# Kernel tuning notes

Measured on AMD Instinct MI355X. Metric: run time of the kernel, lower is better.

Reference implementation:

```python
import jax, jax.numpy as jnp
import numpy as np

N_HEAD = 16
N_EMBD = 1024

def setup_inputs() -> dict:
    key = jax.random.key(0)
    ks = jax.random.split(key, 5)
    C = N_EMBD
    x = jax.random.normal(ks[0], (4, 2048, C), dtype=jnp.float32)
    s = 1.0 / np.sqrt(C)
    W_attn = jax.random.normal(ks[1], (C, 3 * C), dtype=jnp.float32) * s
    b_attn = jax.random.normal(ks[2], (3 * C,), dtype=jnp.float32) * 0.02
    W_proj = jax.random.normal(ks[3], (C, C), dtype=jnp.float32) * s
    b_proj = jax.random.normal(ks[4], (C,), dtype=jnp.float32) * 0.02
    return {"x": x, "W_attn": W_attn, "b_attn": b_attn, "W_proj": W_proj, "b_proj": b_proj}

def reference(x, W_attn, b_attn, W_proj, b_proj):
    B, T, C = x.shape
    H = C // N_HEAD
    qkv = x @ W_attn + b_attn  # [B,T,3C]
    q, k, v = jnp.split(qkv, 3, axis=2)
    # [B,T,C] -> [B,nh,T,H]
    q = q.reshape(B, T, N_HEAD, H).transpose(0, 2, 1, 3)
    k = k.reshape(B, T, N_HEAD, H).transpose(0, 2, 1, 3)
    v = v.reshape(B, T, N_HEAD, H).transpose(0, 2, 1, 3)
    att = jnp.einsum('bhqd,bhkd->bhqk', q, k) * (1.0 / np.sqrt(H).astype(np.float32))
    causal = jnp.tril(jnp.ones((T, T), dtype=bool))  # [T,T]
    att = jnp.where(causal, att, -jnp.inf)
    att = jax.nn.softmax(att, axis=-1)
    y = jnp.einsum('bhqk,bhkd->bhqd', att, v)
    y = y.transpose(0, 2, 1, 3).reshape(B, T, C)
    return y @ W_proj + b_proj
```

## Files before the change

kernel.cpp:

```cpp
#include <hip/hip_runtime.h>
#include <math.h>

#define T_LEN 2048
#define C_DIM 1024
#define C3    3072
#define NHEAD 16
#define HDIM  64

typedef __attribute__((ext_vector_type(8))) __bf16 bf16x8;
typedef __attribute__((ext_vector_type(8))) unsigned short u16x8;
typedef __attribute__((ext_vector_type(4))) float f32x4;
typedef __attribute__((ext_vector_type(2))) unsigned int u32x2;
typedef unsigned short ushort_t;

#define QK_SCALE 0.180336878f

#if defined(__has_builtin)
#if __has_builtin(__builtin_amdgcn_exp2f)
#define FAST_EXP2(x) __builtin_amdgcn_exp2f(x)
#endif
#if __has_builtin(__builtin_amdgcn_permlane32_swap) && __has_builtin(__builtin_amdgcn_permlane16_swap)
#define HAVE_PERMLANE_SWAP 1
#endif
#endif
#ifndef FAST_EXP2
#define FAST_EXP2(x) exp2f(x)
#endif

__device__ __forceinline__ ushort_t f2bf(float f) {
    unsigned int u = __float_as_uint(f);
    unsigned int r = (u + 0x7FFFu + ((u >> 16) & 1u)) >> 16;
    return (ushort_t)r;
}

#define GLL16(g, l) __builtin_amdgcn_global_load_lds( \
    (const __attribute__((address_space(1))) void*)(g), \
    (__attribute__((address_space(3))) void*)(l), 16, 0, 0)

__global__ __launch_bounds__(256) void prep_inputs(
    const float* __restrict__ x, ushort_t* __restrict__ xb,
    const float* __restrict__ W1, ushort_t* __restrict__ Wt1,
    const float* __restrict__ W2, ushort_t* __restrict__ Wt2)
{
    __shared__ float t[64][65];
    const int bx = blockIdx.x;
    if (bx < 8192) {
        const int i = bx * 256 + threadIdx.x;
        const float4 v = ((const float4*)x)[i];
        ushort4 o;
        o.x = f2bf(v.x); o.y = f2bf(v.y); o.z = f2bf(v.z); o.w = f2bf(v.w);
        ((ushort4*)xb)[i] = o;
        return;
    }
    const float* W; ushort_t* Wt; int N, n0, k0;
    if (bx < 8960) {
        const int tt = bx - 8192;
        W = W1; Wt = Wt1; N = C3;
        n0 = (tt % 48) * 64; k0 = (tt / 48) * 64;
    } else {
        const int tt = bx - 8960;
        W = W2; Wt = Wt2; N = C_DIM;
        n0 = (tt % 16) * 64; k0 = (tt / 16) * 64;
    }
    const int K = C_DIM;
    const int c = threadIdx.x & 63, r4 = threadIdx.x >> 6;
#pragma unroll
    for (int i = 0; i < 16; i++) {
        int r = i * 4 + r4;
        t[r][c] = W[(size_t)(k0 + r) * N + n0 + c];
    }
    __syncthreads();
#pragma unroll
    for (int i = 0; i < 16; i++) {
        int r = i * 4 + r4;
        Wt[(size_t)(n0 + r) * K + k0 + c] = f2bf(t[c][r]);
    }
}

template <bool OUT_BF16, bool QSCALE>
__global__ __launch_bounds__(256, 3) void gemm_bt_mfma(
    const ushort_t* __restrict__ A, const ushort_t* __restrict__ Bt,
    const float* __restrict__ bias, void* __restrict__ Cv,
    int M, int N, int K)
{
    __shared__ ushort_t Alds[128 * 64];
    __shared__ ushort_t Blds[128 * 64];

    const int tid = threadIdx.x;
    const int m0 = blockIdx.y * 128;
    const int n0 = blockIdx.x * 128;
    const int w = tid >> 6;
    const int ln = tid & 63;
    const int quad = ln >> 4;
    const int r16 = ln & 15;
    const int wr0 = (w & 1) * 64;
    const int wc0 = (w >> 1) * 64;

    f32x4 acc[4][4] = {};

    const int srow = tid >> 3;
    const int csrc8 = ((tid & 7) ^ (srow & 7)) * 8;
    const int sw = r16 & 7;

    for (int k0 = 0; k0 < K; k0 += 64) {
#pragma unroll
        for (int rr = 0; rr < 4; rr++) {
            const ushort_t* ga = A + (size_t)(m0 + rr * 32 + srow) * K + k0 + csrc8;
            GLL16(ga, Alds + rr * 2048 + tid * 8);
            const ushort_t* gb = Bt + (size_t)(n0 + rr * 32 + srow) * K + k0 + csrc8;
            GLL16(gb, Blds + rr * 2048 + tid * 8);
        }
        __syncthreads();

#pragma unroll
        for (int s = 0; s < 2; s++) {
            const int cpos = ((4 * s + quad) ^ sw) * 8;
            bf16x8 af[4], bfr[4];
#pragma unroll
            for (int i = 0; i < 4; i++)
                af[i] = *(const bf16x8*)(Alds + (wr0 + i * 16 + r16) * 64 + cpos);
#pragma unroll
            for (int j = 0; j < 4; j++)
                bfr[j] = *(const bf16x8*)(Blds + (wc0 + j * 16 + r16) * 64 + cpos);
#pragma unroll
            for (int i = 0; i < 4; i++)
#pragma unroll
                for (int j = 0; j < 4; j++)
                    acc[i][j] = __builtin_amdgcn_mfma_f32_16x16x32_bf16(
                        af[i], bfr[j], acc[i][j], 0, 0, 0);
        }
        __syncthreads();
    }

    const float scl = (QSCALE && n0 < C_DIM) ? QK_SCALE : 1.0f;

#pragma unroll
    for (int j = 0; j < 4; j++) {
        const int col = n0 + wc0 + j * 16 + r16;
        const float bv = bias[col];
#pragma unroll
        for (int i = 0; i < 4; i++) {
            const int rowb = m0 + wr0 + i * 16 + quad * 4;
#pragma unroll
            for (int r = 0; r < 4; r++) {
                const float v = (acc[i][j][r] + bv) * scl;
                if (OUT_BF16)
                    ((ushort_t*)Cv)[(size_t)(rowb + r) * N + col] = f2bf(v);
                else
                    ((float*)Cv)[(size_t)(rowb + r) * N + col] = v;
            }
        }
    }
}

__global__ __launch_bounds__(256) void transpose_v(
    const ushort_t* __restrict__ qkv, ushort_t* __restrict__ vtg)
{
    __shared__ ushort_t Ts[64][72];
    const int t0 = blockIdx.x * 64;
    const int bh = blockIdx.y;
    const int b = bh >> 4, h = bh & 15;
    const ushort_t* src = qkv + (size_t)b * T_LEN * C3 + 2 * C_DIM + h * HDIM;
    const int tid = threadIdx.x;
    {
        const int r = tid >> 2, cs = (tid & 3) * 16;
        *(u16x8*)(&Ts[r][cs])     = *(const u16x8*)(src + (size_t)(t0 + r) * C3 + cs);
        *(u16x8*)(&Ts[r][cs + 8]) = *(const u16x8*)(src + (size_t)(t0 + r) * C3 + cs + 8);
    }
    __syncthreads();
    {
        const int d = tid >> 2, ts0 = (tid & 3) * 16;
        ushort_t* dst = vtg + ((size_t)bh * HDIM + d) * T_LEN + t0 + ts0;
        u16x8 o0, o1;
#pragma unroll
        for (int j = 0; j < 8; j++) o0[j] = Ts[ts0 + j][d];
#pragma unroll
        for (int j = 0; j < 8; j++) o1[j] = Ts[ts0 + 8 + j][d];
        *(u16x8*)dst = o0;
        *(u16x8*)(dst + 8) = o1;
    }
}


__device__ __forceinline__ void mask_diag(f32x4 (&s)[4], int qloc, int quad)
{
#pragma unroll
    for (int mb = 0; mb < 4; mb++)
#pragma unroll
        for (int r = 0; r < 4; r++)
            if (mb * 16 + quad * 4 + r > qloc) s[mb][r] = -1e30f;
}

__device__ __forceinline__ void softmax_exchange(
    f32x4 (&s)[4], float& lacc, bf16x8 (&bp)[2])
{
    unsigned int pk[4][2];
#pragma unroll
    for (int mb = 0; mb < 4; mb++) {
        const float p0 = FAST_EXP2(s[mb][0]);
        const float p1 = FAST_EXP2(s[mb][1]);
        const float p2 = FAST_EXP2(s[mb][2]);
        const float p3 = FAST_EXP2(s[mb][3]);
        lacc += (p0 + p1) + (p2 + p3);
        pk[mb][0] = __builtin_amdgcn_perm(__float_as_uint(p1), __float_as_uint(p0), 0x07060302u);
        pk[mb][1] = __builtin_amdgcn_perm(__float_as_uint(p3), __float_as_uint(p2), 0x07060302u);
    }
#pragma unroll
    for (int s2 = 0; s2 < 2; s2++) {
        uint4 t;
#pragma unroll
        for (int u = 0; u < 2; u++) {
            unsigned int A = pk[2 * s2][u], B = pk[2 * s2 + 1][u];
            unsigned int out1, out2;
#ifdef HAVE_PERMLANE_SWAP
            u32x2 r1 = __builtin_amdgcn_permlane32_swap(A, B, false, false);
            u32x2 r2 = __builtin_amdgcn_permlane16_swap(r1.x, r1.y, false, false);
            out1 = r2.x; out2 = r2.y;
#else
            asm volatile("s_nop 1\n\t"
                         "v_permlane32_swap_b32 %0, %1\n\t"
                         "s_nop 1\n\t"
                         "v_permlane16_swap_b32 %0, %1"
                         : "+v"(A), "+v"(B));
            out1 = A; out2 = B;
#endif
            if (u == 0) { t.x = out1; t.z = out2; }
            else        { t.y = out1; t.w = out2; }
        }
        bp[s2] = *(bf16x8*)&t;
    }
}

#define STAGE_K(kt_, buf_) do {                                               \
    const int _k0 = (kt_) * 64;                                               \
    const int _bo = (buf_) * 4096;                                            \
    _Pragma("unroll")                                                         \
    for (int rr = 0; rr < 2; rr++) {                                          \
        const ushort_t* gk = basek + (size_t)(_k0 + rr * 32 + srow) * C3 + csrc8; \
        GLL16(gk, Ks + _bo + rr * 2048 + tid * 8);                            \
    }                                                                         \
} while (0)

#define STAGE_V(kt_, buf_) do {                                               \
    const int _k0 = (kt_) * 64;                                               \
    const int _bo = (buf_) * 4096;                                            \
    _Pragma("unroll")                                                         \
    for (int rr = 0; rr < 2; rr++) {                                          \
        const ushort_t* gv = vrow + (size_t)(rr * 32 + srow) * T_LEN + _k0 + csrc8; \
        GLL16(gv, Vs + _bo + rr * 2048 + tid * 8);                            \
    }                                                                         \
} while (0)

__global__ __launch_bounds__(256, 4) void attn_flash_mfma5(
    const ushort_t* __restrict__ qkv, const ushort_t* __restrict__ vtg,
    ushort_t* __restrict__ y)
{
    __shared__ ushort_t Ks[2 * 64 * 64];
    __shared__ ushort_t Vs[2 * 64 * 64];

    const int bid = blockIdx.x;
    const int i = (bid >> 3) >> 3;
    const int bh = (bid & 7) * 8 + ((bid >> 3) & 7);
    const int b = bh >> 4, h = bh & 15;
    const int qA0 = i * 64;
    const int qB0 = (31 - i) * 64;
    const int lastkt = 31 - i;

    const int tid = threadIdx.x;
    const int w = tid >> 6;
    const int ln = tid & 63;
    const int quad = ln >> 4;
    const int r16 = ln & 15;
    const int qloc = w * 16 + r16;
    const int sw = r16 & 7;

    const int srow = tid >> 3;
    const int csrc8 = ((tid & 7) ^ (srow & 7)) * 8;
    const int cpos0 = (quad ^ sw) * 8;

    const ushort_t* baseq = qkv + (size_t)b * T_LEN * C3 + h * HDIM;
    const ushort_t* basek = baseq + C_DIM;
    const ushort_t* vrow = vtg + (size_t)bh * HDIM * T_LEN;

    STAGE_K(0, 0);
    STAGE_V(0, 0);

    bf16x8 aqA[2], aqB[2];
#pragma unroll
    for (int s = 0; s < 2; s++) {
        aqA[s] = *(const bf16x8*)(baseq + (size_t)(qA0 + qloc) * C3 + s * 32 + quad * 8);
        aqB[s] = *(const bf16x8*)(baseq + (size_t)(qB0 + qloc) * C3 + s * 32 + quad * 8);
    }

    f32x4 oA[4] = {}, oB[4] = {};
    float lA = 0.0f, lB = 0.0f;

    for (int kt = 0; kt <= lastkt; kt++) {
        __syncthreads();

        if (kt < lastkt) {
            STAGE_K(kt + 1, (kt + 1) & 1);
            STAGE_V(kt + 1, (kt + 1) & 1);
        }

        const int kb = (kt & 1) * 4096;

        if (kt <= i) {
            f32x4 sA[4] = {}, sB[4] = {};
#pragma unroll
            for (int s = 0; s < 2; s++)
#pragma unroll
                for (int mb = 0; mb < 4; mb++) {
                    const bf16x8 ak = *(const bf16x8*)(Ks + kb + (mb * 16 + r16) * 64 + (cpos0 ^ (s * 32)));
                    sA[mb] = __builtin_amdgcn_mfma_f32_16x16x32_bf16(ak, aqA[s], sA[mb], 0, 0, 0);
                    sB[mb] = __builtin_amdgcn_mfma_f32_16x16x32_bf16(ak, aqB[s], sB[mb], 0, 0, 0);
                }
            if (kt == i) mask_diag(sA, qloc, quad);
            bf16x8 bpA[2], bpB[2];
            softmax_exchange(sA, lA, bpA);
            softmax_exchange(sB, lB, bpB);
#pragma unroll
            for (int s = 0; s < 2; s++)
#pragma unroll
                for (int mb = 0; mb < 4; mb++) {
                    const bf16x8 av = *(const bf16x8*)(Vs + kb + (mb * 16 + r16) * 64 + (cpos0 ^ (s * 32)));
                    oA[mb] = __builtin_amdgcn_mfma_f32_16x16x32_bf16(av, bpA[s], oA[mb], 0, 0, 0);
                    oB[mb] = __builtin_amdgcn_mfma_f32_16x16x32_bf16(av, bpB[s], oB[mb], 0, 0, 0);
                }
        } else {
            f32x4 sB[4] = {};
#pragma unroll
            for (int s = 0; s < 2; s++)
#pragma unroll
                for (int mb = 0; mb < 4; mb++) {
                    const bf16x8 ak = *(const bf16x8*)(Ks + kb + (mb * 16 + r16) * 64 + (cpos0 ^ (s * 32)));
                    sB[mb] = __builtin_amdgcn_mfma_f32_16x16x32_bf16(ak, aqB[s], sB[mb], 0, 0, 0);
                }
            if (kt == lastkt) mask_diag(sB, qloc, quad);
            bf16x8 bpB[2];
            softmax_exchange(sB, lB, bpB);
#pragma unroll
            for (int s = 0; s < 2; s++)
#pragma unroll
                for (int mb = 0; mb < 4; mb++) {
                    const bf16x8 av = *(const bf16x8*)(Vs + kb + (mb * 16 + r16) * 64 + (cpos0 ^ (s * 32)));
                    oB[mb] = __builtin_amdgcn_mfma_f32_16x16x32_bf16(av, bpB[s], oB[mb], 0, 0, 0);
                }
        }
    }

    lA += __shfl_xor(lA, 16); lA += __shfl_xor(lA, 32);
    lB += __shfl_xor(lB, 16); lB += __shfl_xor(lB, 32);
    {
        const float invA = 1.0f / lA;
        ushort_t* yp = y + ((size_t)(b * T_LEN + qA0 + qloc)) * C_DIM + h * HDIM;
#pragma unroll
        for (int mb = 0; mb < 4; mb++) {
            ushort4 o;
            o.x = f2bf(oA[mb][0] * invA);
            o.y = f2bf(oA[mb][1] * invA);
            o.z = f2bf(oA[mb][2] * invA);
            o.w = f2bf(oA[mb][3] * invA);
            *(ushort4*)(yp + mb * 16 + quad * 4) = o;
        }
    }
    {
        const float invB = 1.0f / lB;
        ushort_t* yp = y + ((size_t)(b * T_LEN + qB0 + qloc)) * C_DIM + h * HDIM;
#pragma unroll
        for (int mb = 0; mb < 4; mb++) {
            ushort4 o;
            o.x = f2bf(oB[mb][0] * invB);
            o.y = f2bf(oB[mb][1] * invB);
            o.z = f2bf(oB[mb][2] * invB);
            o.w = f2bf(oB[mb][3] * invB);
            *(ushort4*)(yp + mb * 16 + quad * 4) = o;
        }
    }
}

extern "C" void kernel_launch(void* const* d_in, const int* in_sizes, int n_in,
                              void* d_out, int out_size, void* d_ws, size_t ws_size,
                              hipStream_t stream)
{
    const float* x      = (const float*)d_in[0];
    const float* W_attn = (const float*)d_in[1];
    const float* b_attn = (const float*)d_in[2];
    const float* W_proj = (const float*)d_in[3];
    const float* b_proj = (const float*)d_in[4];
    float* out = (float*)d_out;

    const int M = 4 * T_LEN;
    char* ws = (char*)d_ws;
    ushort_t* qkv = (ushort_t*)ws;
    ushort_t* xb  = (ushort_t*)(ws + 50331648);
    ushort_t* Wt1 = (ushort_t*)(ws + 67108864);
    ushort_t* yb  = (ushort_t*)(ws + 73400320);
    ushort_t* Wt2 = (ushort_t*)(ws + 90177536);
    ushort_t* vtg = (ushort_t*)(ws + 92274688);

    prep_inputs<<<9216, 256, 0, stream>>>(x, xb, W_attn, Wt1, W_proj, Wt2);

    gemm_bt_mfma<true, true><<<dim3(C3 / 128, M / 128), 256, 0, stream>>>(
        xb, Wt1, b_attn, qkv, M, C3, C_DIM);

    transpose_v<<<dim3(T_LEN / 64, 4 * NHEAD), 256, 0, stream>>>(qkv, vtg);

    attn_flash_mfma5<<<dim3(1024), 256, 0, stream>>>(qkv, vtg, yb);

    gemm_bt_mfma<false, false><<<dim3(C_DIM / 128, M / 128), 256, 0, stream>>>(
        yb, Wt2, b_proj, out, M, C_DIM, C_DIM);
}
```

Baseline: 255.5 us.

## Load K/V fragments directly from global into registers, drop LDS staging

Removes shared-memory double buffering and block-wide barriers in the flash attention kernel. Each wave now loads its K and V MFMA operand fragments straight from global memory into registers, with K prefetched one tile ahead in a ping-pong register pair. Occupancy hint drops from 4 to 2 blocks per CU to make room for the extra registers. Trade-off: each of the 4 waves redundantly fetches the same K/V tile (4x more global/L2 traffic) and V loads are not prefetched, so their latency is exposed before the PV MFMAs.

```diff
diff --git a/kernel.cpp b/kernel.cpp
--- a/kernel.cpp
+++ b/kernel.cpp
@@ -231,40 +231,86 @@
     }
 }
 
-#define STAGE_K(kt_, buf_) do {                                               \
-    const int _k0 = (kt_) * 64;                                               \
-    const int _bo = (buf_) * 4096;                                            \
-    _Pragma("unroll")                                                         \
-    for (int rr = 0; rr < 2; rr++) {                                          \
-        const ushort_t* gk = basek + (size_t)(_k0 + rr * 32 + srow) * C3 + csrc8; \
-        GLL16(gk, Ks + _bo + rr * 2048 + tid * 8);                            \
-    }                                                                         \
-} while (0)
-
-#define STAGE_V(kt_, buf_) do {                                               \
-    const int _k0 = (kt_) * 64;                                               \
-    const int _bo = (buf_) * 4096;                                            \
-    _Pragma("unroll")                                                         \
-    for (int rr = 0; rr < 2; rr++) {                                          \
-        const ushort_t* gv = vrow + (size_t)(rr * 32 + srow) * T_LEN + _k0 + csrc8; \
-        GLL16(gv, Vs + _bo + rr * 2048 + tid * 8);                            \
-    }                                                                         \
-} while (0)
-
-__global__ __launch_bounds__(256, 4) void attn_flash_mfma5(
+struct AttnCtx {
+    const ushort_t* basek;
+    const ushort_t* vrow;
+    int i, lastkt, qloc, quad, r16, dq;
+    bf16x8 aqA[2], aqB[2];
+    f32x4 oA[4], oB[4];
+    float lA, lB;
+};
+
+__device__ __forceinline__ void issue_k(AttnCtx& c, bf16x8 (&kf)[2][4], int kt)
+{
+    const ushort_t* p = c.basek + (size_t)(kt * 64 + c.r16) * C3 + c.dq;
+#pragma unroll
+    for (int s = 0; s < 2; s++)
+#pragma unroll
+        for (int mb = 0; mb < 4; mb++)
+            kf[s][mb] = *(const bf16x8*)(p + (size_t)(mb * 16) * C3 + s * 32);
+}
+
+__device__ __forceinline__ void issue_v(AttnCtx& c, bf16x8 (&vf)[2][4], int kt)
+{
+    const ushort_t* p = c.vrow + (size_t)c.r16 * T_LEN + kt * 64 + c.dq;
+#pragma unroll
+    for (int s = 0; s < 2; s++)
+#pragma unroll
+        for (int mb = 0; mb < 4; mb++)
+            vf[s][mb] = *(const bf16x8*)(p + (size_t)(mb * 16) * T_LEN + s * 32);
+}
+
+__device__ __forceinline__ void attn_body(
+    AttnCtx& c, const bf16x8 (&kf)[2][4], const bf16x8 (&vf)[2][4], int kt)
+{
+    if (kt <= c.i) {
+        f32x4 sA[4] = {}, sB[4] = {};
+#pragma unroll
+        for (int s = 0; s < 2; s++)
+#pragma unroll
+            for (int mb = 0; mb < 4; mb++) {
+                sA[mb] = __builtin_amdgcn_mfma_f32_16x16x32_bf16(kf[s][mb], c.aqA[s], sA[mb], 0, 0, 0);
+                sB[mb] = __builtin_amdgcn_mfma_f32_16x16x32_bf16(kf[s][mb], c.aqB[s], sB[mb], 0, 0, 0);
+            }
+        if (kt == c.i) mask_diag(sA, c.qloc, c.quad);
+        bf16x8 bpA[2], bpB[2];
+        softmax_exchange(sA, c.lA, bpA);
+        softmax_exchange(sB, c.lB, bpB);
+#pragma unroll
+        for (int s = 0; s < 2; s++)
+#pragma unroll
+            for (int mb = 0; mb < 4; mb++) {
+                c.oA[mb] = __builtin_amdgcn_mfma_f32_16x16x32_bf16(vf[s][mb], bpA[s], c.oA[mb], 0, 0, 0);
+                c.oB[mb] = __builtin_amdgcn_mfma_f32_16x16x32_bf16(vf[s][mb], bpB[s], c.oB[mb], 0, 0, 0);
+            }
+    } else {
+        f32x4 sB[4] = {};
+#pragma unroll
+        for (int s = 0; s < 2; s++)
+#pragma unroll
+            for (int mb = 0; mb < 4; mb++)
+                sB[mb] = __builtin_amdgcn_mfma_f32_16x16x32_bf16(kf[s][mb], c.aqB[s], sB[mb], 0, 0, 0);
+        if (kt == c.lastkt) mask_diag(sB, c.qloc, c.quad);
+        bf16x8 bpB[2];
+        softmax_exchange(sB, c.lB, bpB);
+#pragma unroll
+        for (int s = 0; s < 2; s++)
+#pragma unroll
+            for (int mb = 0; mb < 4; mb++)
+                c.oB[mb] = __builtin_amdgcn_mfma_f32_16x16x32_bf16(vf[s][mb], bpB[s], c.oB[mb], 0, 0, 0);
+    }
+}
+
+__global__ __launch_bounds__(256, 2) void attn_flash_mfma5(
     const ushort_t* __restrict__ qkv, const ushort_t* __restrict__ vtg,
     ushort_t* __restrict__ y)
 {
-    __shared__ ushort_t Ks[2 * 64 * 64];
-    __shared__ ushort_t Vs[2 * 64 * 64];
-
     const int bid = blockIdx.x;
     const int i = (bid >> 3) >> 3;
     const int bh = (bid & 7) * 8 + ((bid >> 3) & 7);
     const int b = bh >> 4, h = bh & 15;
     const int qA0 = i * 64;
     const int qB0 = (31 - i) * 64;
-    const int lastkt = 31 - i;
 
     const int tid = threadIdx.x;
     const int w = tid >> 6;
@@ -272,83 +318,40 @@
     const int quad = ln >> 4;
     const int r16 = ln & 15;
     const int qloc = w * 16 + r16;
-    const int sw = r16 & 7;
-
-    const int srow = tid >> 3;
-    const int csrc8 = ((tid & 7) ^ (srow & 7)) * 8;
-    const int cpos0 = (quad ^ sw) * 8;
 
     const ushort_t* baseq = qkv + (size_t)b * T_LEN * C3 + h * HDIM;
-    const ushort_t* basek = baseq + C_DIM;
-    const ushort_t* vrow = vtg + (size_t)bh * HDIM * T_LEN;
-
-    STAGE_K(0, 0);
-    STAGE_V(0, 0);
-
-    bf16x8 aqA[2], aqB[2];
+
+    AttnCtx c;
+    c.basek = baseq + C_DIM;
+    c.vrow  = vtg + (size_t)bh * HDIM * T_LEN;
+    c.i = i; c.lastkt = 31 - i;
+    c.qloc = qloc; c.quad = quad; c.r16 = r16; c.dq = quad * 8;
+    c.lA = 0.0f; c.lB = 0.0f;
+#pragma unroll
+    for (int mb = 0; mb < 4; mb++) { c.oA[mb] = (f32x4){}; c.oB[mb] = (f32x4){}; }
+
+    bf16x8 kf0[2][4], kf1[2][4], vf[2][4];
+    issue_k(c, kf0, 0);
 #pragma unroll
     for (int s = 0; s < 2; s++) {
-        aqA[s] = *(const bf16x8*)(baseq + (size_t)(qA0 + qloc) * C3 + s * 32 + quad * 8);
-        aqB[s] = *(const bf16x8*)(baseq + (size_t)(qB0 + qloc) * C3 + s * 32 + quad * 8);
-    }
-
-    f32x4 oA[4] = {}, oB[4] = {};
-    float lA = 0.0f, lB = 0.0f;
-
-    for (int kt = 0; kt <= lastkt; kt++) {
-        __syncthreads();
-
-        if (kt < lastkt) {
-            STAGE_K(kt + 1, (kt + 1) & 1);
-            STAGE_V(kt + 1, (kt + 1) & 1);
-        }
-
-        const int kb = (kt & 1) * 4096;
-
-        if (kt <= i) {
-            f32x4 sA[4] = {}, sB[4] = {};
-#pragma unroll
-            for (int s = 0; s < 2; s++)
-#pragma unroll
-                for (int mb = 0; mb < 4; mb++) {
-                    const bf16x8 ak = *(const bf16x8*)(Ks + kb + (mb * 16 + r16) * 64 + (cpos0 ^ (s * 32)));
-                    sA[mb] = __builtin_amdgcn_mfma_f32_16x16x32_bf16(ak, aqA[s], sA[mb], 0, 0, 0);
-                    sB[mb] = __builtin_amdgcn_mfma_f32_16x16x32_bf16(ak, aqB[s], sB[mb], 0, 0, 0);
-                }
-            if (kt == i) mask_diag(sA, qloc, quad);
-            bf16x8 bpA[2], bpB[2];
-            softmax_exchange(sA, lA, bpA);
-            softmax_exchange(sB, lB, bpB);
-#pragma unroll
-            for (int s = 0; s < 2; s++)
-#pragma unroll
-                for (int mb = 0; mb < 4; mb++) {
-                    const bf16x8 av = *(const bf16x8*)(Vs + kb + (mb * 16 + r16) * 64 + (cpos0 ^ (s * 32)));
-                    oA[mb] = __builtin_amdgcn_mfma_f32_16x16x32_bf16(av, bpA[s], oA[mb], 0, 0, 0);
-                    oB[mb] = __builtin_amdgcn_mfma_f32_16x16x32_bf16(av, bpB[s], oB[mb], 0, 0, 0);
-                }
-        } else {
-            f32x4 sB[4] = {};
-#pragma unroll
-            for (int s = 0; s < 2; s++)
-#pragma unroll
-                for (int mb = 0; mb < 4; mb++) {
-                    const bf16x8 ak = *(const bf16x8*)(Ks + kb + (mb * 16 + r16) * 64 + (cpos0 ^ (s * 32)));
-                    sB[mb] = __builtin_amdgcn_mfma_f32_16x16x32_bf16(ak, aqB[s], sB[mb], 0, 0, 0);
-                }
-            if (kt == lastkt) mask_diag(sB, qloc, quad);
-            bf16x8 bpB[2];
-            softmax_exchange(sB, lB, bpB);
-#pragma unroll
-            for (int s = 0; s < 2; s++)
-#pragma unroll
-                for (int mb = 0; mb < 4; mb++) {
-                    const bf16x8 av = *(const bf16x8*)(Vs + kb + (mb * 16 + r16) * 64 + (cpos0 ^ (s * 32)));
-                    oB[mb] = __builtin_amdgcn_mfma_f32_16x16x32_bf16(av, bpB[s], oB[mb], 0, 0, 0);
-                }
-        }
-    }
-
+        c.aqA[s] = *(const bf16x8*)(baseq + (size_t)(qA0 + qloc) * C3 + s * 32 + c.dq);
+        c.aqB[s] = *(const bf16x8*)(baseq + (size_t)(qB0 + qloc) * C3 + s * 32 + c.dq);
+    }
+
+    int kt = 0;
+    while (true) {
+        if (kt + 1 <= c.lastkt) issue_k(c, kf1, kt + 1);
+        issue_v(c, vf, kt);
+        attn_body(c, kf0, vf, kt);
+        if (++kt > c.lastkt) break;
+
+        if (kt + 1 <= c.lastkt) issue_k(c, kf0, kt + 1);
+        issue_v(c, vf, kt);
+        attn_body(c, kf1, vf, kt);
+        if (++kt > c.lastkt) break;
+    }
+
+    float lA = c.lA, lB = c.lB;
     lA += __shfl_xor(lA, 16); lA += __shfl_xor(lA, 32);
     lB += __shfl_xor(lB, 16); lB += __shfl_xor(lB, 32);
     {
@@ -357,10 +360,10 @@
 #pragma unroll
         for (int mb = 0; mb < 4; mb++) {
             ushort4 o;
-            o.x = f2bf(oA[mb][0] * invA);
-            o.y = f2bf(oA[mb][1] * invA);
-            o.z = f2bf(oA[mb][2] * invA);
-            o.w = f2bf(oA[mb][3] * invA);
+            o.x = f2bf(c.oA[mb][0] * invA);
+            o.y = f2bf(c.oA[mb][1] * invA);
+            o.z = f2bf(c.oA[mb][2] * invA);
+            o.w = f2bf(c.oA[mb][3] * invA);
             *(ushort4*)(yp + mb * 16 + quad * 4) = o;
         }
     }
@@ -370,10 +373,10 @@
 #pragma unroll
         for (int mb = 0; mb < 4; mb++) {
             ushort4 o;
-            o.x = f2bf(oB[mb][0] * invB);
-            o.y = f2bf(oB[mb][1] * invB);
-            o.z = f2bf(oB[mb][2] * invB);
-            o.w = f2bf(oB[mb][3] * invB);
+            o.x = f2bf(c.oB[mb][0] * invB);
+            o.y = f2bf(c.oB[mb][1] * invB);
+            o.z = f2bf(c.oB[mb][2] * invB);
+            o.w = f2bf(c.oB[mb][3] * invB);
             *(ushort4*)(yp + mb * 16 + quad * 4) = o;
         }
     }
```

Result: slower. 379.5 us (+48.5%).
